# Optimization experiments

Hardware: AMD Instinct MI355X
Metric: run time of the kernel (lower is better)

Reference implementation:

```python
import jax, jax.numpy as jnp
import numpy as np


def setup_inputs() -> dict:
    key = jax.random.key(0)
    k1, k2, k3, k4 = jax.random.split(key, 4)
    P, BPP, S, DIN, DOUT, LEVELS = 8, 8, 4096, 256, 256, 7  # parscale_n, batch/path, seq, dims, bit levels (2..8)
    x = jax.random.normal(k1, (P * BPP, S, DIN), dtype=jnp.float32)
    # one dequantized weight per bit level (stand-in for mp_weight.get_weight(bits))
    weight_bank = jax.random.normal(k2, (LEVELS, DOUT, DIN), dtype=jnp.float32) * 0.02
    bias = jax.random.normal(k3, (DOUT,), dtype=jnp.float32) * 0.02
    assigned_bits = jax.random.randint(k4, (P,), 0, LEVELS, dtype=jnp.int64)  # index into weight_bank
    return {"x": x, "weight_bank": weight_bank, "bias": bias, "assigned_bits": assigned_bits}


def reference(x, weight_bank, bias, assigned_bits):
    P = assigned_bits.shape[0]
    B, S, Din = x.shape
    bpp = B // P
    xs = x.reshape(P, bpp, S, Din)                 # [P, bpp, S, Din]
    W = weight_bank[assigned_bits]                 # per-path weight select [P, Dout, Din]
    out = jnp.einsum('pbsi,poi->pbso', xs, W) + bias  # grouped dequant-matmul
    return out.reshape(P * bpp, S, -1)
```

## Files before the change

kernel.cpp:

```cpp
#include <hip/hip_runtime.h>


typedef float  floatx4  __attribute__((ext_vector_type(4)));
typedef short  shortx8  __attribute__((ext_vector_type(8)));
typedef unsigned short ushortx4 __attribute__((ext_vector_type(4)));

constexpr int DIN  = 256;
constexpr int DOUT = 256;
constexpr int ROWS_PER_PATH = 8 * 4096;
constexpr int BM   = 64;
constexpr int WBANK_ELEMS = 7 * DOUT * DIN;

__device__ __forceinline__ unsigned short f2bf(float f) {
  union { float f; unsigned u; } c; c.f = f;
  unsigned r = c.u + 0x7fffu + ((c.u >> 16) & 1u);
  return (unsigned short)(r >> 16);
}

__device__ __forceinline__ shortx8 cvt8(floatx4 v0, floatx4 v1) {
  shortx8 h;
  h[0] = (short)f2bf(v0.x); h[1] = (short)f2bf(v0.y);
  h[2] = (short)f2bf(v0.z); h[3] = (short)f2bf(v0.w);
  h[4] = (short)f2bf(v1.x); h[5] = (short)f2bf(v1.y);
  h[6] = (short)f2bf(v1.z); h[7] = (short)f2bf(v1.w);
  return h;
}

__global__ void convert_w_kernel(const float* __restrict__ w,
                                 unsigned short* __restrict__ o, int n4) {
  int i = blockIdx.x * 256 + threadIdx.x;
  if (i < n4) {
    floatx4 v = ((const floatx4*)w)[i];
    ushortx4 h;
    h.x = f2bf(v.x); h.y = f2bf(v.y); h.z = f2bf(v.z); h.w = f2bf(v.w);
    ((ushortx4*)o)[i] = h;
  }
}

template <bool WBF>
__global__ __launch_bounds__(256, 4)
void mp_linear_kernel(const float* __restrict__ x,
                      const void*  __restrict__ wsel,
                      const float* __restrict__ bias,
                      const int*   __restrict__ bits,
                      float* __restrict__ out) {
  __shared__ short xs[BM * DIN];

  const int tid  = threadIdx.x;
  const int row0 = blockIdx.x * BM;
  const int path = row0 / ROWS_PER_PATH;
  const int widx = bits[path];

  const int lane = tid & 63;
  const int wave = tid >> 6;
  const int n0   = wave * 64;
  const int quad = lane >> 4;
  const int l16  = lane & 15;

  {
    const float* xt = x + (size_t)row0 * DIN;
    floatx4 v[16];
#pragma unroll
    for (int c = 0; c < 8; ++c) {
      const float* p = xt + (size_t)(tid + c * 256) * 8;
      v[2 * c]     = *(const floatx4*)p;
      v[2 * c + 1] = *(const floatx4*)(p + 4);
    }
#pragma unroll
    for (int c = 0; c < 8; ++c) {
      const int g   = tid + c * 256;
      const int row = g >> 5;
      const int col = (g & 31) * 8;
      int byte = (row * DIN + col) * 2;
      byte ^= (row & 7) << 4;
      *(shortx8*)((char*)xs + byte) = cvt8(v[2 * c], v[2 * c + 1]);
    }
  }
  __syncthreads();

  const unsigned short* __restrict__ wbf =
      (const unsigned short*)wsel + (size_t)widx * (DOUT * DIN)
      + (size_t)(n0 + l16) * DIN + quad * 8;
  const float* __restrict__ wf32 =
      (const float*)wsel + (size_t)widx * (DOUT * DIN)
      + (size_t)(n0 + l16) * DIN + quad * 8;

  floatx4 acc[4][4];
#pragma unroll
  for (int i = 0; i < 4; ++i)
#pragma unroll
    for (int j = 0; j < 4; ++j)
      acc[i][j] = (floatx4)0.f;

#pragma unroll 2
  for (int k0 = 0; k0 < DIN; k0 += 32) {
    shortx8 a[4], xf[4];
#pragma unroll
    for (int nf = 0; nf < 4; ++nf) {
      if (WBF) {
        a[nf] = *(const shortx8*)(wbf + (size_t)(nf * 16) * DIN + k0);
      } else {
        const float* p = wf32 + (size_t)(nf * 16) * DIN + k0;
        a[nf] = cvt8(*(const floatx4*)p, *(const floatx4*)(p + 4));
      }
    }
#pragma unroll
    for (int mf = 0; mf < 4; ++mf) {
      const int row = mf * 16 + l16;
      int byte = (row * DIN + k0 + quad * 8) * 2;
      byte ^= (row & 7) << 4;
      xf[mf] = *(const shortx8*)((const char*)xs + byte);
    }
#pragma unroll
    for (int mf = 0; mf < 4; ++mf)
#pragma unroll
      for (int nf = 0; nf < 4; ++nf)
        acc[mf][nf] = __builtin_amdgcn_mfma_f32_16x16x32_bf16(
            a[nf], xf[mf], acc[mf][nf], 0, 0, 0);
  }

  floatx4 bv[4];
#pragma unroll
  for (int nf = 0; nf < 4; ++nf)
    bv[nf] = *(const floatx4*)(bias + n0 + nf * 16 + quad * 4);

#pragma unroll
  for (int mf = 0; mf < 4; ++mf) {
    float* orow = out + (size_t)(row0 + mf * 16 + l16) * DOUT + n0 + quad * 4;
#pragma unroll
    for (int nf = 0; nf < 4; ++nf) {
      floatx4 o4 = acc[mf][nf] + bv[nf];
      *(floatx4*)(orow + nf * 16) = o4;
    }
  }
}

extern "C" void kernel_launch(void* const* d_in, const int* in_sizes, int n_in,
                              void* d_out, int out_size, void* d_ws, size_t ws_size,
                              hipStream_t stream) {
  const float* x     = (const float*)d_in[0];
  const float* wbank = (const float*)d_in[1];
  const float* bias  = (const float*)d_in[2];
  const int*   bits  = (const int*)d_in[3];
  float*       out   = (float*)d_out;

  const int total_rows = in_sizes[0] / DIN;
  const int grid = total_rows / BM;

  const size_t wbf_bytes = (size_t)WBANK_ELEMS * sizeof(unsigned short);
  if (ws_size >= wbf_bytes) {
    unsigned short* wbf = (unsigned short*)d_ws;
    const int n4 = WBANK_ELEMS / 4;
    convert_w_kernel<<<(n4 + 255) / 256, 256, 0, stream>>>(wbank, wbf, n4);
    mp_linear_kernel<true><<<grid, 256, 0, stream>>>(x, wbf, bias, bits, out);
  } else {
    mp_linear_kernel<false><<<grid, 256, 0, stream>>>(x, wbank, bias, bits, out);
  }
}
```

Before: 473.3 us.

## Halve row tile, preload full weight slice into registers, use nontemporal stores

Row tile per block goes from 64 to 32. Each wave now loads its entire 64x256 bf16 weight slice into registers before the x tile is converted, so the weight fetch overlaps with the x-to-LDS staging and the MFMA loop has no global loads. Output stores become nontemporal to avoid polluting cache. In exchange the kernel holds many more VGPRs (occupancy hint lowered to 2), and the smaller row tile means the weight slice is fetched twice as often across blocks.

```diff
diff --git a/kernel.cpp b/kernel.cpp
--- a/kernel.cpp
+++ b/kernel.cpp
@@ -8,7 +8,7 @@
 constexpr int DIN  = 256;
 constexpr int DOUT = 256;
 constexpr int ROWS_PER_PATH = 8 * 4096;
-constexpr int BM   = 64;
+constexpr int BM   = 32;
 constexpr int WBANK_ELEMS = 7 * DOUT * DIN;
 
 __device__ __forceinline__ unsigned short f2bf(float f) {
@@ -38,7 +38,7 @@
 }
 
 template <bool WBF>
-__global__ __launch_bounds__(256, 4)
+__global__ __launch_bounds__(256, 2)
 void mp_linear_kernel(const float* __restrict__ x,
                       const void*  __restrict__ wsel,
                       const float* __restrict__ bias,
@@ -57,66 +57,73 @@
   const int quad = lane >> 4;
   const int l16  = lane & 15;
 
-  {
-    const float* xt = x + (size_t)row0 * DIN;
-    floatx4 v[16];
+  const float* xt = x + (size_t)row0 * DIN;
+  floatx4 v[8];
 #pragma unroll
-    for (int c = 0; c < 8; ++c) {
-      const float* p = xt + (size_t)(tid + c * 256) * 8;
-      v[2 * c]     = *(const floatx4*)p;
-      v[2 * c + 1] = *(const floatx4*)(p + 4);
-    }
+  for (int c = 0; c < 4; ++c) {
+    const float* p = xt + (size_t)(tid + c * 256) * 8;
+    v[2 * c]     = *(const floatx4*)p;
+    v[2 * c + 1] = *(const floatx4*)(p + 4);
+  }
+
+  shortx8 w[4][8];
+  if (WBF) {
+    const unsigned short* __restrict__ wp =
+        (const unsigned short*)wsel + (size_t)widx * (DOUT * DIN)
+        + (size_t)(n0 + l16) * DIN + quad * 8;
 #pragma unroll
-    for (int c = 0; c < 8; ++c) {
-      const int g   = tid + c * 256;
-      const int row = g >> 5;
-      const int col = (g & 31) * 8;
-      int byte = (row * DIN + col) * 2;
-      byte ^= (row & 7) << 4;
-      *(shortx8*)((char*)xs + byte) = cvt8(v[2 * c], v[2 * c + 1]);
-    }
+    for (int nf = 0; nf < 4; ++nf)
+#pragma unroll
+      for (int kk = 0; kk < 8; ++kk)
+        w[nf][kk] = *(const shortx8*)(wp + (size_t)(nf * 16) * DIN + kk * 32);
+  } else {
+    const float* __restrict__ wp =
+        (const float*)wsel + (size_t)widx * (DOUT * DIN)
+        + (size_t)(n0 + l16) * DIN + quad * 8;
+#pragma unroll
+    for (int nf = 0; nf < 4; ++nf)
+#pragma unroll
+      for (int kk = 0; kk < 8; ++kk) {
+        const float* p = wp + (size_t)(nf * 16) * DIN + kk * 32;
+        w[nf][kk] = cvt8(*(const floatx4*)p, *(const floatx4*)(p + 4));
+      }
+  }
+
+#pragma unroll
+  for (int c = 0; c < 4; ++c) {
+    const int g   = tid + c * 256;
+    const int row = g >> 5;
+    const int col = (g & 31) * 8;
+    int byte = (row * DIN + col) * 2;
+    byte ^= (row & 7) << 4;
+    *(shortx8*)((char*)xs + byte) = cvt8(v[2 * c], v[2 * c + 1]);
   }
   __syncthreads();
 
-  const unsigned short* __restrict__ wbf =
-      (const unsigned short*)wsel + (size_t)widx * (DOUT * DIN)
-      + (size_t)(n0 + l16) * DIN + quad * 8;
-  const float* __restrict__ wf32 =
-      (const float*)wsel + (size_t)widx * (DOUT * DIN)
-      + (size_t)(n0 + l16) * DIN + quad * 8;
-
-  floatx4 acc[4][4];
+  floatx4 acc[2][4];
 #pragma unroll
-  for (int i = 0; i < 4; ++i)
+  for (int i = 0; i < 2; ++i)
 #pragma unroll
     for (int j = 0; j < 4; ++j)
       acc[i][j] = (floatx4)0.f;
 
-#pragma unroll 2
-  for (int k0 = 0; k0 < DIN; k0 += 32) {
-    shortx8 a[4], xf[4];
 #pragma unroll
-    for (int nf = 0; nf < 4; ++nf) {
-      if (WBF) {
-        a[nf] = *(const shortx8*)(wbf + (size_t)(nf * 16) * DIN + k0);
-      } else {
-        const float* p = wf32 + (size_t)(nf * 16) * DIN + k0;
-        a[nf] = cvt8(*(const floatx4*)p, *(const floatx4*)(p + 4));
-      }
-    }
+  for (int kk = 0; kk < 8; ++kk) {
+    const int k0 = kk * 32;
+    shortx8 xf[2];
 #pragma unroll
-    for (int mf = 0; mf < 4; ++mf) {
+    for (int mf = 0; mf < 2; ++mf) {
       const int row = mf * 16 + l16;
       int byte = (row * DIN + k0 + quad * 8) * 2;
       byte ^= (row & 7) << 4;
       xf[mf] = *(const shortx8*)((const char*)xs + byte);
     }
 #pragma unroll
-    for (int mf = 0; mf < 4; ++mf)
+    for (int mf = 0; mf < 2; ++mf)
 #pragma unroll
       for (int nf = 0; nf < 4; ++nf)
         acc[mf][nf] = __builtin_amdgcn_mfma_f32_16x16x32_bf16(
-            a[nf], xf[mf], acc[mf][nf], 0, 0, 0);
+            w[nf][kk], xf[mf], acc[mf][nf], 0, 0, 0);
   }
 
   floatx4 bv[4];
@@ -125,12 +132,12 @@
     bv[nf] = *(const floatx4*)(bias + n0 + nf * 16 + quad * 4);
 
 #pragma unroll
-  for (int mf = 0; mf < 4; ++mf) {
+  for (int mf = 0; mf < 2; ++mf) {
     float* orow = out + (size_t)(row0 + mf * 16 + l16) * DOUT + n0 + quad * 4;
 #pragma unroll
     for (int nf = 0; nf < 4; ++nf) {
       floatx4 o4 = acc[mf][nf] + bv[nf];
-      *(floatx4*)(orow + nf * 16) = o4;
+      __builtin_nontemporal_store(o4, (floatx4*)(orow + nf * 16));
     }
   }
 }
```

After: 513.7 us. +8.5%, slower.
